# Kernel optimization log

Hardware: AMD Instinct MI355X
Metric: run time of the kernel (lower is better)

Reference implementation:

```python
import jax, jax.numpy as jnp
import numpy as np

B, IN, H = 4096, 2048, 2048


def setup_inputs() -> dict:
    key = jax.random.key(0)
    ks = jax.random.split(key, 20)
    s_in = 1.0 / np.sqrt(IN)
    s_h = 1.0 / np.sqrt(H)
    inp = {
        "x": jax.random.normal(ks[0], (B, IN), jnp.float32),
        "h": jax.random.normal(ks[1], (B, H), jnp.float32),
        "c": jax.random.normal(ks[2], (B, H), jnp.float32),
    }
    names_in = [("Wii", "bii"), ("Wif", "bif"), ("Wig", "big"), ("Wio", "bio")]
    names_h = [("Whi", "bhi"), ("Whf", "bhf"), ("Whg", "bhg"), ("Who", "bho")]
    k = 3
    for wn, bn in names_in:
        inp[wn] = jax.random.normal(ks[k], (H, IN), jnp.float32) * s_in
        inp[bn] = jax.random.normal(ks[k + 1], (H,), jnp.float32) * s_in
        k += 2
    for wn, bn in names_h:
        inp[wn] = jax.random.normal(ks[k], (H, H), jnp.float32) * s_h
        inp[bn] = jax.random.normal(ks[k + 1], (H,), jnp.float32) * s_h
        k += 2
    return inp


def reference(x, h, c, Wii, bii, Whi, bhi, Wif, bif, Whf, bhf,
              Wig, big, Whg, bhg, Wio, bio, Who, bho):
    # Fuse the 4 input-projections and 4 hidden-projections into two GEMMs
    # (same math as 8 separate nn.Linear calls).
    Wx = jnp.concatenate([Wii, Wif, Wig, Wio], axis=0)   # [4H, IN]
    Wh = jnp.concatenate([Whi, Whf, Whg, Who], axis=0)   # [4H, H]
    bx = jnp.concatenate([bii, bif, big, bio])            # [4H]
    bh = jnp.concatenate([bhi, bhf, bhg, bho])            # [4H]
    gates = x @ Wx.T + h @ Wh.T + bx + bh                 # [B, 4H]
    ii, ff, gg, oo = jnp.split(gates, 4, axis=-1)
    i = jax.nn.sigmoid(ii)
    f = jax.nn.sigmoid(ff)
    g = jnp.tanh(gg)
    o = jax.nn.sigmoid(oo)
    c_new = f * c + i * g
    h_new = o * jnp.tanh(c_new)
    return jnp.stack([h_new, c_new])  # [2, B, H]
```

## Files before the change

### kernel.cpp

```cpp
#include <hip/hip_runtime.h>
#include <stdint.h>

typedef __attribute__((ext_vector_type(4))) float f32x4;
typedef __attribute__((ext_vector_type(8))) short bf16x8;

#define MFMA_BF16 __builtin_amdgcn_mfma_f32_16x16x32_bf16

__device__ __forceinline__ unsigned short f2bf(float f) {
  union { float f; uint32_t u; } a; a.f = f;
  uint32_t u = a.u;
  uint32_t r = (u + 0x7FFFu + ((u >> 16) & 1u)) >> 16;
  return (unsigned short)r;
}

__global__ void pack_a_kernel(const float4* __restrict__ x, const float4* __restrict__ hh,
                              ushort4* __restrict__ A) {
  const int total = 4096 * 1024;
  for (int q = blockIdx.x * blockDim.x + threadIdx.x; q < total; q += gridDim.x * blockDim.x) {
    int row = q >> 10, cq = q & 1023;
    float4 v = (cq < 512) ? x[row * 512 + cq] : hh[row * 512 + (cq - 512)];
    ushort4 o; o.x = f2bf(v.x); o.y = f2bf(v.y); o.z = f2bf(v.z); o.w = f2bf(v.w);
    A[q] = o;
  }
}

__global__ void pack_w_kernel(const float* __restrict__ Wii, const float* __restrict__ Wif,
                              const float* __restrict__ Wig, const float* __restrict__ Wio,
                              const float* __restrict__ Whi, const float* __restrict__ Whf,
                              const float* __restrict__ Whg, const float* __restrict__ Who,
                              ushort4* __restrict__ Wp) {
  const int total = 8192 * 1024;
  for (int q = blockIdx.x * blockDim.x + threadIdx.x; q < total; q += gridDim.x * blockDim.x) {
    int p = q >> 10, kq = q & 1023;
    int r = p & 255;
    int g = ((r >> 7) << 1) | ((r >> 4) & 1);
    int H = ((p >> 8) << 6) | (((r >> 5) & 3) << 4) | (r & 15);
    const float* src;
    if (kq < 512) src = (g == 0) ? Wii : (g == 1) ? Wif : (g == 2) ? Wig : Wio;
    else          src = (g == 0) ? Whi : (g == 1) ? Whf : (g == 2) ? Whg : Who;
    const float4 v = *(const float4*)&src[(size_t)H * 2048 + ((kq & 511) << 2)];
    ushort4 o; o.x = f2bf(v.x); o.y = f2bf(v.y); o.z = f2bf(v.z); o.w = f2bf(v.w);
    Wp[q] = o;
  }
}

#define STG(srcbase, jj, koff, dstE)                                                        \
  __builtin_amdgcn_global_load_lds(                                                        \
      (const __attribute__((address_space(1))) void*)((srcbase) + (size_t)(jj)*262144 + (koff)), \
      (__attribute__((address_space(3))) void*)(&smem[(dstE) + (jj)*4096]), 16, 0, 0)

__global__ __launch_bounds__(512, 1)
void lstm_gemm_kernel(const ushort* __restrict__ A, const ushort* __restrict__ Wp,
                      const float* __restrict__ c,
                      const float* __restrict__ bii, const float* __restrict__ bif_,
                      const float* __restrict__ big_, const float* __restrict__ bio_,
                      const float* __restrict__ bhi, const float* __restrict__ bhf,
                      const float* __restrict__ bhg, const float* __restrict__ bho,
                      float* __restrict__ out) {
  __shared__ ushort smem[65536];
  const int tid = threadIdx.x;
  const int lane = tid & 63, w = tid >> 6;
  const int wm = w >> 2, wn = w & 3;

  const int bid = blockIdx.x;
  const int wg = (bid & 7) * 64 + (bid >> 3);
  const int bm = wg >> 5, bn = wg & 31;

  const int laneRow = lane & 15, lane16 = lane >> 4;
  const int lr7 = laneRow & 7;
  const int colE0 = (lane16 ^ lr7) << 3;
  const int colE1 = ((4 + lane16) ^ lr7) << 3;

  const int srow = w * 8 + (lane >> 3);
  const int chunkOff = ((lane & 7) ^ (lane >> 3)) << 3;
  const ushort* aSrc = A + (size_t)(bm * 256 + srow) * 4096 + chunkOff;
  const ushort* bSrc = Wp + (size_t)(bn * 256 + srow) * 4096 + chunkOff;
  const int aDstW = w * 512;
  const int bDstW = 16384 + w * 512;

  const int aBase = (wm * 64 + laneRow) * 64;
  const int bBase = 16384 + (wn * 32 + laneRow) * 64;

  f32x4 acc[8][4];
#pragma unroll
  for (int i = 0; i < 8; i++)
#pragma unroll
    for (int j = 0; j < 4; j++) acc[i][j] = (f32x4){0.f, 0.f, 0.f, 0.f};

  STG(aSrc, 0, 0, aDstW); STG(aSrc, 1, 0, aDstW);
  STG(bSrc, 0, 0, bDstW); STG(bSrc, 1, 0, bDstW);
  STG(aSrc, 2, 0, aDstW); STG(aSrc, 3, 0, aDstW);
  STG(bSrc, 2, 0, bDstW); STG(bSrc, 3, 0, bDstW);
  STG(aSrc, 0, 64, 32768 + aDstW); STG(aSrc, 1, 64, 32768 + aDstW);
  STG(bSrc, 0, 64, 32768 + bDstW); STG(bSrc, 1, 64, 32768 + bDstW);
  asm volatile("s_waitcnt vmcnt(8)" ::: "memory");
  __builtin_amdgcn_s_barrier();
  __builtin_amdgcn_sched_barrier(0);

#pragma unroll 1
  for (int T = 0; T < 64; ++T) {
    const int bufE = (T & 1) << 15;
    const int obufE = bufE ^ 32768;
    const int kN = (T + 1) << 6;
    const int kN2 = (T + 2) << 6;
    bf16x8 af[4][2], bf[4][2];

#pragma unroll
    for (int m = 0; m < 4; ++m) {
      af[m][0] = *(const bf16x8*)&smem[bufE + aBase + m * 1024 + colE0];
      af[m][1] = *(const bf16x8*)&smem[bufE + aBase + m * 1024 + colE1];
    }
#pragma unroll
    for (int n = 0; n < 2; ++n) {
      bf[n][0] = *(const bf16x8*)&smem[bufE + bBase + n * 1024 + colE0];
      bf[n][1] = *(const bf16x8*)&smem[bufE + bBase + n * 1024 + colE1];
    }
    if (T < 63) { STG(aSrc, 2, kN, obufE + aDstW); STG(aSrc, 3, kN, obufE + aDstW); }
    __builtin_amdgcn_s_barrier();
    asm volatile("s_waitcnt lgkmcnt(0)" ::: "memory");
    __builtin_amdgcn_sched_barrier(0);
    __builtin_amdgcn_s_setprio(1);
#pragma unroll
    for (int m = 0; m < 4; ++m)
#pragma unroll
      for (int n = 0; n < 2; ++n) {
        acc[m][n] = MFMA_BF16(af[m][0], bf[n][0], acc[m][n], 0, 0, 0);
        acc[m][n] = MFMA_BF16(af[m][1], bf[n][1], acc[m][n], 0, 0, 0);
      }
    __builtin_amdgcn_s_setprio(0);
    if (T < 63) asm volatile("s_waitcnt vmcnt(6)" ::: "memory");
    else        asm volatile("s_waitcnt vmcnt(0)" ::: "memory");
    __builtin_amdgcn_s_barrier();

#pragma unroll
    for (int n = 0; n < 2; ++n) {
      bf[2 + n][0] = *(const bf16x8*)&smem[bufE + bBase + 8192 + n * 1024 + colE0];
      bf[2 + n][1] = *(const bf16x8*)&smem[bufE + bBase + 8192 + n * 1024 + colE1];
    }
    if (T < 63) { STG(bSrc, 2, kN, obufE + bDstW); STG(bSrc, 3, kN, obufE + bDstW); }
    __builtin_amdgcn_s_barrier();
    asm volatile("s_waitcnt lgkmcnt(0)" ::: "memory");
    __builtin_amdgcn_sched_barrier(0);
    __builtin_amdgcn_s_setprio(1);
#pragma unroll
    for (int m = 0; m < 4; ++m)
#pragma unroll
      for (int n = 0; n < 2; ++n) {
        acc[m][2 + n] = MFMA_BF16(af[m][0], bf[2 + n][0], acc[m][2 + n], 0, 0, 0);
        acc[m][2 + n] = MFMA_BF16(af[m][1], bf[2 + n][1], acc[m][2 + n], 0, 0, 0);
      }
    __builtin_amdgcn_s_setprio(0);
    __builtin_amdgcn_s_barrier();

#pragma unroll
    for (int m = 0; m < 4; ++m) {
      af[m][0] = *(const bf16x8*)&smem[bufE + aBase + 8192 + m * 1024 + colE0];
      af[m][1] = *(const bf16x8*)&smem[bufE + aBase + 8192 + m * 1024 + colE1];
    }
    if (T < 62) { STG(aSrc, 0, kN2, bufE + aDstW); STG(aSrc, 1, kN2, bufE + aDstW); }
    __builtin_amdgcn_s_barrier();
    asm volatile("s_waitcnt lgkmcnt(0)" ::: "memory");
    __builtin_amdgcn_sched_barrier(0);
    __builtin_amdgcn_s_setprio(1);
#pragma unroll
    for (int m = 0; m < 4; ++m)
#pragma unroll
      for (int n = 0; n < 2; ++n) {
        acc[4 + m][n] = MFMA_BF16(af[m][0], bf[n][0], acc[4 + m][n], 0, 0, 0);
        acc[4 + m][n] = MFMA_BF16(af[m][1], bf[n][1], acc[4 + m][n], 0, 0, 0);
      }
    __builtin_amdgcn_s_setprio(0);
    __builtin_amdgcn_s_barrier();

    if (T < 62) { STG(bSrc, 0, kN2, bufE + bDstW); STG(bSrc, 1, kN2, bufE + bDstW); }
    __builtin_amdgcn_s_barrier();
    __builtin_amdgcn_s_setprio(1);
#pragma unroll
    for (int m = 0; m < 4; ++m)
#pragma unroll
      for (int n = 0; n < 2; ++n) {
        acc[4 + m][2 + n] = MFMA_BF16(af[m][0], bf[2 + n][0], acc[4 + m][2 + n], 0, 0, 0);
        acc[4 + m][2 + n] = MFMA_BF16(af[m][1], bf[2 + n][1], acc[4 + m][2 + n], 0, 0, 0);
      }
    __builtin_amdgcn_s_setprio(0);
    if (T < 62)      asm volatile("s_waitcnt vmcnt(8)" ::: "memory");
    else if (T == 62) asm volatile("s_waitcnt vmcnt(4)" ::: "memory");
    __builtin_amdgcn_s_barrier();
  }

  const int hcol = bn * 64 + wn * 16 + laneRow;
  const float bI = bii[hcol] + bhi[hcol];
  const float bF = bif_[hcol] + bhf[hcol];
  const float bG = big_[hcol] + bhg[hcol];
  const float bO = bio_[hcol] + bho[hcol];
#pragma unroll
  for (int mi = 0; mi < 8; ++mi) {
    const int rowBase = bm * 256 + (mi >> 2) * 128 + wm * 64 + (mi & 3) * 16 + lane16 * 4;
#pragma unroll
    for (int rr = 0; rr < 4; ++rr) {
      const int row = rowBase + rr;
      const float ii = acc[mi][0][rr] + bI;
      const float ff = acc[mi][1][rr] + bF;
      const float gg = acc[mi][2][rr] + bG;
      const float oo = acc[mi][3][rr] + bO;
      const float iv = 1.f / (1.f + __expf(-ii));
      const float fv = 1.f / (1.f + __expf(-ff));
      const float gv = tanhf(gg);
      const float ov = 1.f / (1.f + __expf(-oo));
      const float cv = c[(size_t)row * 2048 + hcol];
      const float cn = fv * cv + iv * gv;
      const float hn = ov * tanhf(cn);
      out[(size_t)row * 2048 + hcol] = hn;
      out[(size_t)8388608 + (size_t)row * 2048 + hcol] = cn;
    }
  }
}

extern "C" void kernel_launch(void* const* d_in, const int* in_sizes, int n_in,
                              void* d_out, int out_size, void* d_ws, size_t ws_size,
                              hipStream_t stream) {
  const float* x = (const float*)d_in[0];
  const float* h = (const float*)d_in[1];
  const float* c = (const float*)d_in[2];
  const float* Wii = (const float*)d_in[3];  const float* bii = (const float*)d_in[4];
  const float* Wif = (const float*)d_in[5];  const float* bif_ = (const float*)d_in[6];
  const float* Wig = (const float*)d_in[7];  const float* big_ = (const float*)d_in[8];
  const float* Wio = (const float*)d_in[9];  const float* bio_ = (const float*)d_in[10];
  const float* Whi = (const float*)d_in[11]; const float* bhi = (const float*)d_in[12];
  const float* Whf = (const float*)d_in[13]; const float* bhf = (const float*)d_in[14];
  const float* Whg = (const float*)d_in[15]; const float* bhg = (const float*)d_in[16];
  const float* Who = (const float*)d_in[17]; const float* bho = (const float*)d_in[18];

  ushort* Abf = (ushort*)d_ws;
  ushort* Wpk = Abf + (size_t)4096 * 4096;
  float* out = (float*)d_out;

  pack_a_kernel<<<2048, 256, 0, stream>>>((const float4*)x, (const float4*)h, (ushort4*)Abf);
  pack_w_kernel<<<2048, 256, 0, stream>>>(Wii, Wif, Wig, Wio, Whi, Whf, Whg, Who, (ushort4*)Wpk);
  lstm_gemm_kernel<<<512, 512, 0, stream>>>(Abf, Wpk, c,
                                            bii, bif_, big_, bio_, bhi, bhf, bhg, bho, out);
}
```

Measured before the change: 330.6 us.

## Deepen global-to-LDS prefetch to two full tiles and remap blocks per XCD

The prologue now preloads both K-tiles fully, and the loop refills the current buffer for tile T+2 in stages after each quarter of it has been consumed. This keeps more global loads in flight and adjusts the vmcnt waits to match. Block-to-tile mapping is also changed so each XCD owns a contiguous range of weight columns (bn) and sweeps over bm, aiming for better L2 reuse of the weight panels. The risk is that the vmcnt bookkeeping has to be exactly right, or a race or stall follows.

```diff
diff --git a/kernel.cpp b/kernel.cpp
--- a/kernel.cpp
+++ b/kernel.cpp
@@ -63,8 +63,9 @@
   const int wm = w >> 2, wn = w & 3;
 
   const int bid = blockIdx.x;
-  const int wg = (bid & 7) * 64 + (bid >> 3);
-  const int bm = wg >> 5, bn = wg & 31;
+  const int xcd = bid & 7, q = bid >> 3;
+  const int bn = (xcd << 2) | (q >> 4);
+  const int bm = q & 15;
 
   const int laneRow = lane & 15, lane16 = lane >> 4;
   const int lr7 = laneRow & 7;
@@ -89,20 +90,21 @@
 
   STG(aSrc, 0, 0, aDstW); STG(aSrc, 1, 0, aDstW);
   STG(bSrc, 0, 0, bDstW); STG(bSrc, 1, 0, bDstW);
+  STG(bSrc, 2, 0, bDstW); STG(bSrc, 3, 0, bDstW);
   STG(aSrc, 2, 0, aDstW); STG(aSrc, 3, 0, aDstW);
-  STG(bSrc, 2, 0, bDstW); STG(bSrc, 3, 0, bDstW);
   STG(aSrc, 0, 64, 32768 + aDstW); STG(aSrc, 1, 64, 32768 + aDstW);
   STG(bSrc, 0, 64, 32768 + bDstW); STG(bSrc, 1, 64, 32768 + bDstW);
-  asm volatile("s_waitcnt vmcnt(8)" ::: "memory");
+  STG(bSrc, 2, 64, 32768 + bDstW); STG(bSrc, 3, 64, 32768 + bDstW);
+  STG(aSrc, 2, 64, 32768 + aDstW); STG(aSrc, 3, 64, 32768 + aDstW);
+  asm volatile("s_waitcnt vmcnt(12)" ::: "memory");
   __builtin_amdgcn_s_barrier();
   __builtin_amdgcn_sched_barrier(0);
 
 #pragma unroll 1
   for (int T = 0; T < 64; ++T) {
     const int bufE = (T & 1) << 15;
-    const int obufE = bufE ^ 32768;
-    const int kN = (T + 1) << 6;
-    const int kN2 = (T + 2) << 6;
+    const int kS = (T + 2) << 6;
+    const bool st = (T <= 61);
     bf16x8 af[4][2], bf[4][2];
 
 #pragma unroll
@@ -115,7 +117,6 @@
       bf[n][0] = *(const bf16x8*)&smem[bufE + bBase + n * 1024 + colE0];
       bf[n][1] = *(const bf16x8*)&smem[bufE + bBase + n * 1024 + colE1];
     }
-    if (T < 63) { STG(aSrc, 2, kN, obufE + aDstW); STG(aSrc, 3, kN, obufE + aDstW); }
     __builtin_amdgcn_s_barrier();
     asm volatile("s_waitcnt lgkmcnt(0)" ::: "memory");
     __builtin_amdgcn_sched_barrier(0);
@@ -128,8 +129,8 @@
         acc[m][n] = MFMA_BF16(af[m][1], bf[n][1], acc[m][n], 0, 0, 0);
       }
     __builtin_amdgcn_s_setprio(0);
-    if (T < 63) asm volatile("s_waitcnt vmcnt(6)" ::: "memory");
-    else        asm volatile("s_waitcnt vmcnt(0)" ::: "memory");
+    if (T != 63) asm volatile("s_waitcnt vmcnt(10)" ::: "memory");
+    else         asm volatile("s_waitcnt vmcnt(2)" ::: "memory");
     __builtin_amdgcn_s_barrier();
 
 #pragma unroll
@@ -137,7 +138,10 @@
       bf[2 + n][0] = *(const bf16x8*)&smem[bufE + bBase + 8192 + n * 1024 + colE0];
       bf[2 + n][1] = *(const bf16x8*)&smem[bufE + bBase + 8192 + n * 1024 + colE1];
     }
-    if (T < 63) { STG(bSrc, 2, kN, obufE + bDstW); STG(bSrc, 3, kN, obufE + bDstW); }
+    if (st) {
+      STG(aSrc, 0, kS, bufE + aDstW); STG(aSrc, 1, kS, bufE + aDstW);
+      STG(bSrc, 0, kS, bufE + bDstW); STG(bSrc, 1, kS, bufE + bDstW);
+    }
     __builtin_amdgcn_s_barrier();
     asm volatile("s_waitcnt lgkmcnt(0)" ::: "memory");
     __builtin_amdgcn_sched_barrier(0);
@@ -150,6 +154,8 @@
         acc[m][2 + n] = MFMA_BF16(af[m][1], bf[2 + n][1], acc[m][2 + n], 0, 0, 0);
       }
     __builtin_amdgcn_s_setprio(0);
+    if (T != 63) asm volatile("s_waitcnt vmcnt(12)" ::: "memory");
+    else         asm volatile("s_waitcnt vmcnt(0)" ::: "memory");
     __builtin_amdgcn_s_barrier();
 
 #pragma unroll
@@ -157,7 +163,7 @@
       af[m][0] = *(const bf16x8*)&smem[bufE + aBase + 8192 + m * 1024 + colE0];
       af[m][1] = *(const bf16x8*)&smem[bufE + aBase + 8192 + m * 1024 + colE1];
     }
-    if (T < 62) { STG(aSrc, 0, kN2, bufE + aDstW); STG(aSrc, 1, kN2, bufE + aDstW); }
+    if (st) { STG(bSrc, 2, kS, bufE + bDstW); STG(bSrc, 3, kS, bufE + bDstW); }
     __builtin_amdgcn_s_barrier();
     asm volatile("s_waitcnt lgkmcnt(0)" ::: "memory");
     __builtin_amdgcn_sched_barrier(0);
@@ -172,7 +178,7 @@
     __builtin_amdgcn_s_setprio(0);
     __builtin_amdgcn_s_barrier();
 
-    if (T < 62) { STG(bSrc, 0, kN2, bufE + bDstW); STG(bSrc, 1, kN2, bufE + bDstW); }
+    if (st) { STG(aSrc, 2, kS, bufE + aDstW); STG(aSrc, 3, kS, bufE + aDstW); }
     __builtin_amdgcn_s_barrier();
     __builtin_amdgcn_s_setprio(1);
 #pragma unroll
@@ -183,9 +189,12 @@
         acc[4 + m][2 + n] = MFMA_BF16(af[m][1], bf[2 + n][1], acc[4 + m][2 + n], 0, 0, 0);
       }
     __builtin_amdgcn_s_setprio(0);
-    if (T < 62)      asm volatile("s_waitcnt vmcnt(8)" ::: "memory");
-    else if (T == 62) asm volatile("s_waitcnt vmcnt(4)" ::: "memory");
-    __builtin_amdgcn_s_barrier();
+    if (T < 63) {
+      if (T != 62) asm volatile("s_waitcnt vmcnt(12)" ::: "memory");
+      else         asm volatile("s_waitcnt vmcnt(4)" ::: "memory");
+      __builtin_amdgcn_s_barrier();
+      __builtin_amdgcn_sched_barrier(0);
+    }
   }
 
   const int hcol = bn * 64 + wn * 16 + laneRow;
```

Result: no change. 334.3 us (+1.1%).

## Simplify GEMM pipeline to one-barrier double buffering and remap tiles per XCD

Applied to the files above, without the earlier changes.

Replaces the four-phase interleaved prefetch schedule, which had several barriers per K-step, with a simpler double-buffer loop. Each iteration issues all next-tile global-to-LDS loads up front, runs all 32 MFMAs, then waits and synchronises once. It also remaps block IDs so each XCD owns a contiguous group of weight column tiles across all row tiles, aiming for better L2 reuse of the weights. The launch bound is raised to two blocks per CU, but 128 KB of LDS per block likely prevents that co-residency. The raised bound still tightens the register budget, which risks spilling the 128-float accumulator, and the coarser waits can expose more load latency.

```diff
diff --git a/kernel.cpp b/kernel.cpp
--- a/kernel.cpp
+++ b/kernel.cpp
@@ -49,7 +49,7 @@
       (const __attribute__((address_space(1))) void*)((srcbase) + (size_t)(jj)*262144 + (koff)), \
       (__attribute__((address_space(3))) void*)(&smem[(dstE) + (jj)*4096]), 16, 0, 0)
 
-__global__ __launch_bounds__(512, 1)
+__global__ __launch_bounds__(512, 2)
 void lstm_gemm_kernel(const ushort* __restrict__ A, const ushort* __restrict__ Wp,
                       const float* __restrict__ c,
                       const float* __restrict__ bii, const float* __restrict__ bif_,
@@ -63,8 +63,9 @@
   const int wm = w >> 2, wn = w & 3;
 
   const int bid = blockIdx.x;
-  const int wg = (bid & 7) * 64 + (bid >> 3);
-  const int bm = wg >> 5, bn = wg & 31;
+  const int xcd = bid & 7, q = bid >> 3;
+  const int bn = (xcd << 2) | (q >> 4);
+  const int bm = q & 15;
 
   const int laneRow = lane & 15, lane16 = lane >> 4;
   const int lr7 = laneRow & 7;
@@ -88,12 +89,10 @@
     for (int j = 0; j < 4; j++) acc[i][j] = (f32x4){0.f, 0.f, 0.f, 0.f};
 
   STG(aSrc, 0, 0, aDstW); STG(aSrc, 1, 0, aDstW);
+  STG(aSrc, 2, 0, aDstW); STG(aSrc, 3, 0, aDstW);
   STG(bSrc, 0, 0, bDstW); STG(bSrc, 1, 0, bDstW);
-  STG(aSrc, 2, 0, aDstW); STG(aSrc, 3, 0, aDstW);
   STG(bSrc, 2, 0, bDstW); STG(bSrc, 3, 0, bDstW);
-  STG(aSrc, 0, 64, 32768 + aDstW); STG(aSrc, 1, 64, 32768 + aDstW);
-  STG(bSrc, 0, 64, 32768 + bDstW); STG(bSrc, 1, 64, 32768 + bDstW);
-  asm volatile("s_waitcnt vmcnt(8)" ::: "memory");
+  asm volatile("s_waitcnt vmcnt(0)" ::: "memory");
   __builtin_amdgcn_s_barrier();
   __builtin_amdgcn_sched_barrier(0);
 
@@ -101,10 +100,16 @@
   for (int T = 0; T < 64; ++T) {
     const int bufE = (T & 1) << 15;
     const int obufE = bufE ^ 32768;
-    const int kN = (T + 1) << 6;
-    const int kN2 = (T + 2) << 6;
-    bf16x8 af[4][2], bf[4][2];
-
+    const int kS = (T + 1) << 6;
+
+    if (T < 63) {
+      STG(aSrc, 0, kS, obufE + aDstW); STG(aSrc, 1, kS, obufE + aDstW);
+      STG(aSrc, 2, kS, obufE + aDstW); STG(aSrc, 3, kS, obufE + aDstW);
+      STG(bSrc, 0, kS, obufE + bDstW); STG(bSrc, 1, kS, obufE + bDstW);
+      STG(bSrc, 2, kS, obufE + bDstW); STG(bSrc, 3, kS, obufE + bDstW);
+    }
+
+    bf16x8 af[4][2], b01[2][2], b23[2][2];
 #pragma unroll
     for (int m = 0; m < 4; ++m) {
       af[m][0] = *(const bf16x8*)&smem[bufE + aBase + m * 1024 + colE0];
@@ -112,80 +117,62 @@
     }
 #pragma unroll
     for (int n = 0; n < 2; ++n) {
-      bf[n][0] = *(const bf16x8*)&smem[bufE + bBase + n * 1024 + colE0];
-      bf[n][1] = *(const bf16x8*)&smem[bufE + bBase + n * 1024 + colE1];
-    }
-    if (T < 63) { STG(aSrc, 2, kN, obufE + aDstW); STG(aSrc, 3, kN, obufE + aDstW); }
-    __builtin_amdgcn_s_barrier();
-    asm volatile("s_waitcnt lgkmcnt(0)" ::: "memory");
-    __builtin_amdgcn_sched_barrier(0);
-    __builtin_amdgcn_s_setprio(1);
-#pragma unroll
-    for (int m = 0; m < 4; ++m)
-#pragma unroll
-      for (int n = 0; n < 2; ++n) {
-        acc[m][n] = MFMA_BF16(af[m][0], bf[n][0], acc[m][n], 0, 0, 0);
-        acc[m][n] = MFMA_BF16(af[m][1], bf[n][1], acc[m][n], 0, 0, 0);
-      }
-    __builtin_amdgcn_s_setprio(0);
-    if (T < 63) asm volatile("s_waitcnt vmcnt(6)" ::: "memory");
-    else        asm volatile("s_waitcnt vmcnt(0)" ::: "memory");
-    __builtin_amdgcn_s_barrier();
+      b01[n][0] = *(const bf16x8*)&smem[bufE + bBase + n * 1024 + colE0];
+      b01[n][1] = *(const bf16x8*)&smem[bufE + bBase + n * 1024 + colE1];
+    }
+    __builtin_amdgcn_s_setprio(1);
+#pragma unroll
+    for (int m = 0; m < 4; ++m)
+#pragma unroll
+      for (int n = 0; n < 2; ++n) {
+        acc[m][n] = MFMA_BF16(af[m][0], b01[n][0], acc[m][n], 0, 0, 0);
+        acc[m][n] = MFMA_BF16(af[m][1], b01[n][1], acc[m][n], 0, 0, 0);
+      }
+    __builtin_amdgcn_s_setprio(0);
 
 #pragma unroll
     for (int n = 0; n < 2; ++n) {
-      bf[2 + n][0] = *(const bf16x8*)&smem[bufE + bBase + 8192 + n * 1024 + colE0];
-      bf[2 + n][1] = *(const bf16x8*)&smem[bufE + bBase + 8192 + n * 1024 + colE1];
-    }
-    if (T < 63) { STG(bSrc, 2, kN, obufE + bDstW); STG(bSrc, 3, kN, obufE + bDstW); }
-    __builtin_amdgcn_s_barrier();
-    asm volatile("s_waitcnt lgkmcnt(0)" ::: "memory");
-    __builtin_amdgcn_sched_barrier(0);
-    __builtin_amdgcn_s_setprio(1);
-#pragma unroll
-    for (int m = 0; m < 4; ++m)
-#pragma unroll
-      for (int n = 0; n < 2; ++n) {
-        acc[m][2 + n] = MFMA_BF16(af[m][0], bf[2 + n][0], acc[m][2 + n], 0, 0, 0);
-        acc[m][2 + n] = MFMA_BF16(af[m][1], bf[2 + n][1], acc[m][2 + n], 0, 0, 0);
-      }
-    __builtin_amdgcn_s_setprio(0);
-    __builtin_amdgcn_s_barrier();
+      b23[n][0] = *(const bf16x8*)&smem[bufE + bBase + 8192 + n * 1024 + colE0];
+      b23[n][1] = *(const bf16x8*)&smem[bufE + bBase + 8192 + n * 1024 + colE1];
+    }
+    __builtin_amdgcn_s_setprio(1);
+#pragma unroll
+    for (int m = 0; m < 4; ++m)
+#pragma unroll
+      for (int n = 0; n < 2; ++n) {
+        acc[m][2 + n] = MFMA_BF16(af[m][0], b23[n][0], acc[m][2 + n], 0, 0, 0);
+        acc[m][2 + n] = MFMA_BF16(af[m][1], b23[n][1], acc[m][2 + n], 0, 0, 0);
+      }
+    __builtin_amdgcn_s_setprio(0);
 
 #pragma unroll
     for (int m = 0; m < 4; ++m) {
       af[m][0] = *(const bf16x8*)&smem[bufE + aBase + 8192 + m * 1024 + colE0];
       af[m][1] = *(const bf16x8*)&smem[bufE + aBase + 8192 + m * 1024 + colE1];
     }
-    if (T < 62) { STG(aSrc, 0, kN2, bufE + aDstW); STG(aSrc, 1, kN2, bufE + aDstW); }
+    __builtin_amdgcn_s_setprio(1);
+#pragma unroll
+    for (int m = 0; m < 4; ++m)
+#pragma unroll
+      for (int n = 0; n < 2; ++n) {
+        acc[4 + m][n] = MFMA_BF16(af[m][0], b01[n][0], acc[4 + m][n], 0, 0, 0);
+        acc[4 + m][n] = MFMA_BF16(af[m][1], b01[n][1], acc[4 + m][n], 0, 0, 0);
+      }
+    __builtin_amdgcn_s_setprio(0);
+
+    __builtin_amdgcn_s_setprio(1);
+#pragma unroll
+    for (int m = 0; m < 4; ++m)
+#pragma unroll
+      for (int n = 0; n < 2; ++n) {
+        acc[4 + m][2 + n] = MFMA_BF16(af[m][0], b23[n][0], acc[4 + m][2 + n], 0, 0, 0);
+        acc[4 + m][2 + n] = MFMA_BF16(af[m][1], b23[n][1], acc[4 + m][2 + n], 0, 0, 0);
+      }
+    __builtin_amdgcn_s_setprio(0);
+
+    asm volatile("s_waitcnt vmcnt(0)" ::: "memory");
     __builtin_amdgcn_s_barrier();
-    asm volatile("s_waitcnt lgkmcnt(0)" ::: "memory");
     __builtin_amdgcn_sched_barrier(0);
-    __builtin_amdgcn_s_setprio(1);
-#pragma unroll
-    for (int m = 0; m < 4; ++m)
-#pragma unroll
-      for (int n = 0; n < 2; ++n) {
-        acc[4 + m][n] = MFMA_BF16(af[m][0], bf[n][0], acc[4 + m][n], 0, 0, 0);
-        acc[4 + m][n] = MFMA_BF16(af[m][1], bf[n][1], acc[4 + m][n], 0, 0, 0);
-      }
-    __builtin_amdgcn_s_setprio(0);
-    __builtin_amdgcn_s_barrier();
-
-    if (T < 62) { STG(bSrc, 0, kN2, bufE + bDstW); STG(bSrc, 1, kN2, bufE + bDstW); }
-    __builtin_amdgcn_s_barrier();
-    __builtin_amdgcn_s_setprio(1);
-#pragma unroll
-    for (int m = 0; m < 4; ++m)
-#pragma unroll
-      for (int n = 0; n < 2; ++n) {
-        acc[4 + m][2 + n] = MFMA_BF16(af[m][0], bf[2 + n][0], acc[4 + m][2 + n], 0, 0, 0);
-        acc[4 + m][2 + n] = MFMA_BF16(af[m][1], bf[2 + n][1], acc[4 + m][2 + n], 0, 0, 0);
-      }
-    __builtin_amdgcn_s_setprio(0);
-    if (T < 62)      asm volatile("s_waitcnt vmcnt(8)" ::: "memory");
-    else if (T == 62) asm volatile("s_waitcnt vmcnt(4)" ::: "memory");
-    __builtin_amdgcn_s_barrier();
   }
 
   const int hcol = bn * 64 + wn * 16 + laneRow;
```

After: 315.7 us. -4.5%, faster.
